# Kernel tuning notes

Hardware: AMD Instinct MI355X
Metric: run time of the kernel (lower is better)

## Reference

```python
import jax, jax.numpy as jnp
import numpy as np

S = 7                # feature map size
A = 12               # anchors per cell
N = S * S * A        # 588 total anchors
ANCHOR_SCALES = [0.3, 0.5, 0.7, 0.9]
ANCHOR_RATIOS = [0.7, 1.0, 1.3]
CONF_THR = 0.3
NMS_THR = 0.5
MAX_DET = 100
BN_EPS = 1e-5
DN = ('NCHW', 'OIHW', 'NCHW')


def _anchors():
    g = (jnp.arange(S, dtype=jnp.float32) + 0.5) / S
    cx, cy = jnp.meshgrid(g, g, indexing='ij')
    centers = jnp.stack([cx, cy], -1).reshape(-1, 2)                 # [49,2]
    sc = jnp.asarray(ANCHOR_SCALES, jnp.float32)[:, None]
    rt = jnp.sqrt(jnp.asarray(ANCHOR_RATIOS, jnp.float32))[None, :]
    ws = (sc * rt).reshape(-1)
    hs = (sc / rt).reshape(-1)
    deltas = jnp.stack([-ws, -hs, ws, hs], -1) * 0.5                 # [12,4]
    return (jnp.concatenate([centers, centers], -1)[:, None, :] + deltas[None]).reshape(-1, 4)


def _conv(x, w, b, pad):
    y = jax.lax.conv_general_dilated(x, w, (1, 1), [(pad, pad), (pad, pad)], dimension_numbers=DN)
    return y + b[None, :, None, None]


def _bn_relu(x, g, be, mu, var):
    inv = g * jax.lax.rsqrt(var + BN_EPS)
    return jax.nn.relu(x * inv[None, :, None, None] + (be - mu * inv)[None, :, None, None])


def _decode(box_pred, anchors):
    ac = (anchors[:, :2] + anchors[:, 2:]) * 0.5
    asz = anchors[:, 2:] - anchors[:, :2]
    pc = box_pred[..., :2] * asz + ac
    ps = jnp.exp(box_pred[..., 2:]) * asz
    return jnp.concatenate([pc - ps * 0.5, pc + ps * 0.5], -1)


def _iou(b):
    area = (b[:, 2] - b[:, 0]) * (b[:, 3] - b[:, 1])
    lt = jnp.maximum(b[:, None, :2], b[None, :, :2])
    rb = jnp.minimum(b[:, None, 2:], b[None, :, 2:])
    wh = jnp.clip(rb - lt, 0.0)
    inter = wh[..., 0] * wh[..., 1]
    return inter / (area[:, None] + area[None, :] - inter + 1e-9)


def _nms_single(boxes, scores):
    # greedy NMS, fixed-shape: sort by score, sequentially suppress, pad to MAX_DET
    order = jnp.argsort(-scores)
    bs = boxes[order]
    ss = scores[order]
    vs = ss > CONF_THR
    iou = _iou(bs)
    idx = jnp.arange(N)

    def body(suppr, i):
        keep = vs[i] & jnp.logical_not(suppr[i])
        suppr = suppr | (keep & (iou[i] > NMS_THR) & (idx > i))
        return suppr, keep

    _, keep = jax.lax.scan(body, jnp.zeros((N,), bool), idx)
    kept = jnp.where(keep, ss, -1.0)           # scores in (0,1), -1 is a safe sentinel
    top_s, top_i = jax.lax.top_k(kept, MAX_DET)
    valid = top_s > 0.0
    out_b = jnp.where(valid[:, None], bs[top_i], 0.0)
    out_s = jnp.where(valid, top_s, 0.0)
    return jnp.concatenate([out_b, out_s[:, None], valid.astype(jnp.float32)[:, None]], -1)


def _forward(features, w1, b1, g1, be1, mu1, var1, w2, b2, g2, be2, mu2, var2,
             w3, b3, g3, be3, mu3, var3, w4, b4, g4, be4, mu4, var4,
             w_cls, b_cls, w_box, b_box):
    x = _bn_relu(_conv(features, w1, b1, 0), g1, be1, mu1, var1)   # fpn 1x1
    x = _bn_relu(_conv(x, w2, b2, 1), g2, be2, mu2, var2)          # fpn 3x3
    x = _bn_relu(_conv(x, w3, b3, 1), g3, be3, mu3, var3)          # det_conv 1
    x = _bn_relu(_conv(x, w4, b4, 1), g4, be4, mu4, var4)          # det_conv 2
    B = features.shape[0]
    box = _conv(x, w_box, b_box, 1).transpose(0, 2, 3, 1).reshape(B, -1, 4)
    conf = jax.nn.sigmoid(_conv(x, w_cls, b_cls, 1)).transpose(0, 2, 3, 1).reshape(B, -1)
    boxes = _decode(box, _anchors())
    return jax.vmap(_nms_single)(boxes, conf)   # [B, MAX_DET, 6] = box(4)+score+valid


def setup_inputs() -> dict:
    key = jax.random.key(0)
    ks = iter(jax.random.split(key, 64))
    B = 256
    d = {'features': jax.random.normal(next(ks), (B, 512, S, S), jnp.float32)}
    for n, o, i, k in [('1', 256, 512, 1), ('2', 256, 256, 3), ('3', 256, 256, 3), ('4', 256, 256, 3)]:
        d['w' + n] = 0.01 * jax.random.normal(next(ks), (o, i, k, k), jnp.float32)
        d['b' + n] = jnp.zeros((o,), jnp.float32)
        d['g' + n] = 1.0 + 0.1 * jax.random.normal(next(ks), (o,), jnp.float32)
        d['be' + n] = 0.05 * jax.random.normal(next(ks), (o,), jnp.float32)
        d['mu' + n] = 0.1 * jax.random.normal(next(ks), (o,), jnp.float32)
        d['var' + n] = jax.random.uniform(next(ks), (o,), jnp.float32, 0.5, 1.5)
    d['w_cls'] = 0.01 * jax.random.normal(next(ks), (A, 256, 3, 3), jnp.float32)
    d['b_cls'] = jnp.zeros((A,), jnp.float32)
    d['w_box'] = 0.01 * jax.random.normal(next(ks), (4 * A, 256, 3, 3), jnp.float32)
    d['b_box'] = jnp.zeros((4 * A,), jnp.float32)
    return d


def reference(features, w1, b1, g1, be1, mu1, var1, w2, b2, g2, be2, mu2, var2,
              w3, b3, g3, be3, mu3, var3, w4, b4, g4, be4, mu4, var4,
              w_cls, b_cls, w_box, b_box):
    return _forward(features, w1, b1, g1, be1, mu1, var1, w2, b2, g2, be2, mu2, var2,
                    w3, b3, g3, be3, mu3, var3, w4, b4, g4, be4, mu4, var4,
                    w_cls, b_cls, w_box, b_box)
```

## Files before the change

kernel.cpp:

```cpp
#include <hip/hip_runtime.h>
#include <cmath>
#include <cstdint>

#define NPOS 49
#define NANCH 588

__global__ void transpose_all(
    const float* __restrict__ w1, const float* __restrict__ w2,
    const float* __restrict__ w3, const float* __restrict__ w4,
    const float* __restrict__ wb, const float* __restrict__ wc,
    float* __restrict__ w1t, float* __restrict__ w2t, float* __restrict__ w3t,
    float* __restrict__ w4t, float* __restrict__ wbt, float* __restrict__ wct) {
  int idx = blockIdx.x * blockDim.x + threadIdx.x;
  if (idx < 131072) {
    int o = idx / 512, c = idx % 512;
    w1t[((c >> 2) * 256 + o) * 4 + (c & 3)] = w1[idx];
    return;
  }
  idx -= 131072;
  if (idx < 589824) { int o = idx / 2304, ck = idx % 2304; w2t[ck * 256 + o] = w2[idx]; return; }
  idx -= 589824;
  if (idx < 589824) { int o = idx / 2304, ck = idx % 2304; w3t[ck * 256 + o] = w3[idx]; return; }
  idx -= 589824;
  if (idx < 589824) { int o = idx / 2304, ck = idx % 2304; w4t[ck * 256 + o] = w4[idx]; return; }
  idx -= 589824;
  if (idx < 110592) { int o = idx / 2304, ck = idx % 2304; wbt[ck * 48 + o] = wb[idx]; return; }
  idx -= 110592;
  if (idx < 27648)  { int o = idx / 2304, ck = idx % 2304; wct[ck * 12 + o] = wc[idx]; return; }
}

__global__ __launch_bounds__(512, 2) void conv1x1_bn(
    const float* __restrict__ wt_f, const float* __restrict__ in,
    const float* __restrict__ bias, const float* __restrict__ gg,
    const float* __restrict__ be, const float* __restrict__ mu,
    const float* __restrict__ var, float* __restrict__ out) {
  __shared__ float smem[256 * 52];
  const int blk = blockIdx.x, t = threadIdx.x;
  const int b = blk >> 1, oh = blk & 1;
  const int o = t & 127, cg = t >> 7;
  const int og = oh * 128 + o;
  const float* inb = in + (size_t)b * (512 * NPOS);
  const float4* wq = (const float4*)wt_f;
  float acc[NPOS];
#pragma unroll
  for (int p = 0; p < NPOS; ++p) acc[p] = 0.f;
  for (int h = 0; h < 2; ++h) {
    __syncthreads();
    const int q0 = h * 64 + cg * 16;
    float4 wcur = wq[q0 * 256 + og];
    for (int i = t; i < 256 * NPOS; i += 512) {
      int c = i / NPOS, p = i - c * NPOS;
      smem[c * 52 + p] = inb[(h * 256 + c) * NPOS + p];
    }
    __syncthreads();
    for (int q = q0; q < q0 + 16; ++q) {
      int nq = (q + 1 < q0 + 16) ? q + 1 : q;
      float4 wnxt = wq[nq * 256 + og];
      const int clbase = (q - h * 64) * 4;
#pragma unroll
      for (int j = 0; j < 4; ++j) {
        float wv = (j == 0) ? wcur.x : (j == 1) ? wcur.y : (j == 2) ? wcur.z : wcur.w;
        const float4* tr = (const float4*)(smem + (clbase + j) * 52);
#pragma unroll
        for (int jj = 0; jj < 12; ++jj) {
          float4 qv = tr[jj];
          acc[4 * jj + 0] = fmaf(wv, qv.x, acc[4 * jj + 0]);
          acc[4 * jj + 1] = fmaf(wv, qv.y, acc[4 * jj + 1]);
          acc[4 * jj + 2] = fmaf(wv, qv.z, acc[4 * jj + 2]);
          acc[4 * jj + 3] = fmaf(wv, qv.w, acc[4 * jj + 3]);
        }
        acc[48] = fmaf(wv, smem[(clbase + j) * 52 + 48], acc[48]);
      }
      wcur = wnxt;
    }
  }
  __syncthreads();
  float* P0 = smem;
  float* P1 = smem + 6272;
  if (cg == 1) { for (int p = 0; p < NPOS; ++p) P0[o * NPOS + p] = acc[p]; }
  if (cg == 3) { for (int p = 0; p < NPOS; ++p) P1[o * NPOS + p] = acc[p]; }
  __syncthreads();
  if (cg == 0) { for (int p = 0; p < NPOS; ++p) acc[p] += P0[o * NPOS + p]; }
  if (cg == 2) { for (int p = 0; p < NPOS; ++p) acc[p] += P1[o * NPOS + p]; }
  __syncthreads();
  if (cg == 2) { for (int p = 0; p < NPOS; ++p) P0[o * NPOS + p] = acc[p]; }
  __syncthreads();
  if (cg == 0) {
    float scale = gg[og] / sqrtf(var[og] + 1e-5f);
    float add = (bias[og] - mu[og]) * scale + be[og];
#pragma unroll
    for (int p = 0; p < NPOS; ++p) {
      float v = (acc[p] + P0[o * NPOS + p]) * scale + add;
      P1[o * NPOS + p] = v > 0.f ? v : 0.f;
    }
  }
  __syncthreads();
  float* outb = out + (size_t)b * (256 * NPOS) + oh * (128 * NPOS);
  for (int i = t; i < 128 * NPOS; i += 512) outb[i] = P1[i];
}

#define LOADROW(dst, base, rr)                                          \
  do {                                                                  \
    const float4* q4_ = (const float4*)((base) + (rr) * 12);            \
    float4 q0_ = q4_[0], q1_ = q4_[1], q2_ = q4_[2];                    \
    dst[0] = q0_.x; dst[1] = q0_.y; dst[2] = q0_.z; dst[3] = q0_.w;     \
    dst[4] = q1_.x; dst[5] = q1_.y; dst[6] = q1_.z; dst[7] = q1_.w;     \
    dst[8] = q2_.x;                                                     \
  } while (0)

__global__ __launch_bounds__(512, 2) void conv3x3_bn(
    const float* __restrict__ in, const float* __restrict__ wt,
    const float* __restrict__ bias, const float* __restrict__ gg,
    const float* __restrict__ be, const float* __restrict__ mu,
    const float* __restrict__ var, float* __restrict__ out) {
  __shared__ float smem[128 * 108];
  const int blk = blockIdx.x, t = threadIdx.x;
  const int b = blk >> 1, oh = blk & 1;
  const int o = t & 127, cg = t >> 7;
  const int og = oh * 128 + o;
  const float* inb = in + (size_t)b * (256 * NPOS);
  for (int i = t; i < 128 * 108; i += 512) smem[i] = 0.f;
  float acc[NPOS];
#pragma unroll
  for (int p = 0; p < NPOS; ++p) acc[p] = 0.f;
  for (int h = 0; h < 2; ++h) {
    __syncthreads();
    const int cb = h * 128 + cg * 32;
    float wc_[9];
#pragma unroll
    for (int k = 0; k < 9; ++k) wc_[k] = wt[(cb * 9 + k) * 256 + og];
    for (int i = t; i < 128 * NPOS; i += 512) {
      int c = i / NPOS, p = i - c * NPOS, y = p / 7, x = p - y * 7;
      smem[c * 108 + (y + 1) * 12 + (x + 1)] = inb[(h * 128 + c) * NPOS + p];
    }
    __syncthreads();
    for (int cl = 0; cl < 32; ++cl) {
      const int c = cb + cl;
      const int cn = (cl + 1 < 32) ? c + 1 : c;
      float wn_[9];
#pragma unroll
      for (int k = 0; k < 9; ++k) wn_[k] = wt[(cn * 9 + k) * 256 + og];
      const float* tb = smem + (cg * 32 + cl) * 108;
      float R[3][9];
      LOADROW(R[0], tb, 0);
      LOADROW(R[1], tb, 1);
#pragma unroll
      for (int y = 0; y < 7; ++y) {
        LOADROW(R[(y + 2) % 3], tb, y + 2);
        const float* r0 = R[y % 3];
        const float* r1 = R[(y + 1) % 3];
        const float* r2 = R[(y + 2) % 3];
#pragma unroll
        for (int x = 0; x < 7; ++x) {
          float s = acc[y * 7 + x];
          s = fmaf(wc_[0], r0[x], s);
          s = fmaf(wc_[1], r0[x + 1], s);
          s = fmaf(wc_[2], r0[x + 2], s);
          s = fmaf(wc_[3], r1[x], s);
          s = fmaf(wc_[4], r1[x + 1], s);
          s = fmaf(wc_[5], r1[x + 2], s);
          s = fmaf(wc_[6], r2[x], s);
          s = fmaf(wc_[7], r2[x + 1], s);
          s = fmaf(wc_[8], r2[x + 2], s);
          acc[y * 7 + x] = s;
        }
      }
#pragma unroll
      for (int k = 0; k < 9; ++k) wc_[k] = wn_[k];
    }
  }
  __syncthreads();
  float* P0 = smem;
  float* P1 = smem + 6272;
  if (cg == 1) { for (int p = 0; p < NPOS; ++p) P0[o * NPOS + p] = acc[p]; }
  if (cg == 3) { for (int p = 0; p < NPOS; ++p) P1[o * NPOS + p] = acc[p]; }
  __syncthreads();
  if (cg == 0) { for (int p = 0; p < NPOS; ++p) acc[p] += P0[o * NPOS + p]; }
  if (cg == 2) { for (int p = 0; p < NPOS; ++p) acc[p] += P1[o * NPOS + p]; }
  __syncthreads();
  if (cg == 2) { for (int p = 0; p < NPOS; ++p) P0[o * NPOS + p] = acc[p]; }
  __syncthreads();
  if (cg == 0) {
    float scale = gg[og] / sqrtf(var[og] + 1e-5f);
    float add = (bias[og] - mu[og]) * scale + be[og];
#pragma unroll
    for (int p = 0; p < NPOS; ++p) {
      float v = (acc[p] + P0[o * NPOS + p]) * scale + add;
      P1[o * NPOS + p] = v > 0.f ? v : 0.f;
    }
  }
  __syncthreads();
  float* outb = out + (size_t)b * (256 * NPOS) + oh * (128 * NPOS);
  for (int i = t; i < 128 * NPOS; i += 512) outb[i] = P1[i];
}

__global__ __launch_bounds__(512, 2) void heads_decode(
    const float* __restrict__ in, const float* __restrict__ wbt,
    const float* __restrict__ wct, const float* __restrict__ bb,
    const float* __restrict__ bc, float* __restrict__ BXg,
    float* __restrict__ SCg) {
  __shared__ float smem[256 * 108];
  const int b = blockIdx.x, t = threadIdx.x;
  for (int i = t; i < 256 * 108; i += 512) smem[i] = 0.f;
  __syncthreads();
  const float* inb = in + (size_t)b * (256 * NPOS);
  for (int i = t; i < 256 * NPOS; i += 512) {
    int c = i / NPOS, p = i - c * NPOS, y = p / 7, x = p - y * 7;
    smem[c * 108 + (y + 1) * 12 + (x + 1)] = inb[i];
  }
  __syncthreads();
  float acc[NPOS];
#pragma unroll
  for (int p = 0; p < NPOS; ++p) acc[p] = 0.f;
  int o = 0, cg = 0;
  if (t < 480) {
    o = t % 60; cg = t / 60;
    const float* wbase; int wstr;
    if (o < 48) { wbase = wbt + o; wstr = 48; }
    else        { wbase = wct + (o - 48); wstr = 12; }
    const int c0 = cg * 32;
    float wc_[9];
#pragma unroll
    for (int k = 0; k < 9; ++k) wc_[k] = wbase[(c0 * 9 + k) * wstr];
    for (int c = c0; c < c0 + 32; ++c) {
      int cn = (c + 1 < c0 + 32) ? c + 1 : c;
      float wn_[9];
#pragma unroll
      for (int k = 0; k < 9; ++k) wn_[k] = wbase[(cn * 9 + k) * wstr];
      const float* tb = smem + c * 108;
      float R[3][9];
      LOADROW(R[0], tb, 0);
      LOADROW(R[1], tb, 1);
#pragma unroll
      for (int y = 0; y < 7; ++y) {
        LOADROW(R[(y + 2) % 3], tb, y + 2);
        const float* r0 = R[y % 3];
        const float* r1 = R[(y + 1) % 3];
        const float* r2 = R[(y + 2) % 3];
#pragma unroll
        for (int x = 0; x < 7; ++x) {
          float s = acc[y * 7 + x];
          s = fmaf(wc_[0], r0[x], s);
          s = fmaf(wc_[1], r0[x + 1], s);
          s = fmaf(wc_[2], r0[x + 2], s);
          s = fmaf(wc_[3], r1[x], s);
          s = fmaf(wc_[4], r1[x + 1], s);
          s = fmaf(wc_[5], r1[x + 2], s);
          s = fmaf(wc_[6], r2[x], s);
          s = fmaf(wc_[7], r2[x + 1], s);
          s = fmaf(wc_[8], r2[x + 2], s);
          acc[y * 7 + x] = s;
        }
      }
#pragma unroll
      for (int k = 0; k < 9; ++k) wc_[k] = wn_[k];
    }
  }
  __syncthreads();
  float* part = smem;
  float* H = smem + 7 * 2940;
  if (t < 480 && cg > 0) {
#pragma unroll
    for (int p = 0; p < NPOS; ++p) part[(cg - 1) * 2940 + o * NPOS + p] = acc[p];
  }
  __syncthreads();
  if (t < 60) {
    float bsum = (o < 48) ? bb[o] : bc[o - 48];
#pragma unroll
    for (int p = 0; p < NPOS; ++p) {
      float v = acc[p] + bsum;
      for (int g = 0; g < 7; ++g) v += part[g * 2940 + o * NPOS + p];
      H[o * NPOS + p] = v;
    }
  }
  __syncthreads();
  const float scl[4] = {0.3f, 0.5f, 0.7f, 0.9f};
  const float rat[3] = {0.7f, 1.0f, 1.3f};
  for (int n = t; n < NANCH; n += 512) {
    int p = n / 12, a = n - p * 12;
    int ph = p / 7, pw = p - ph * 7;
    float cx = (ph + 0.5f) / 7.0f;
    float cy = (pw + 0.5f) / 7.0f;
    int s = a / 3, r = a - s * 3;
    float rt = sqrtf(rat[r]);
    float wsz = scl[s] * rt, hsz = scl[s] / rt;
    float x1 = cx + (-wsz) * 0.5f, y1 = cy + (-hsz) * 0.5f;
    float x2 = cx + wsz * 0.5f,    y2 = cy + hsz * 0.5f;
    float acx = (x1 + x2) * 0.5f,  acy = (y1 + y2) * 0.5f;
    float asx = x2 - x1,           asy = y2 - y1;
    float bp0 = H[(a * 4 + 0) * NPOS + p];
    float bp1 = H[(a * 4 + 1) * NPOS + p];
    float bp2 = H[(a * 4 + 2) * NPOS + p];
    float bp3 = H[(a * 4 + 3) * NPOS + p];
    float pcx = bp0 * asx + acx;
    float pcy = bp1 * asy + acy;
    float psx = expf(bp2) * asx;
    float psy = expf(bp3) * asy;
    float* bx = BXg + (size_t)b * (NANCH * 4) + n * 4;
    bx[0] = pcx - psx * 0.5f;
    bx[1] = pcy - psy * 0.5f;
    bx[2] = pcx + psx * 0.5f;
    bx[3] = pcy + psy * 0.5f;
    float lg = H[(48 + a) * NPOS + p];
    SCg[(size_t)b * NANCH + n] = 1.0f / (1.0f + expf(-lg));
  }
}

__device__ inline unsigned long long shfl64(unsigned long long v, int lane) {
  int lo = __shfl((int)(unsigned)(v & 0xffffffffULL), lane, 64);
  int hi = __shfl((int)(unsigned)(v >> 32), lane, 64);
  return ((unsigned long long)(unsigned)hi << 32) | (unsigned)lo;
}

__global__ __launch_bounds__(512, 4) void nms_kernel(
    const float* __restrict__ BXg, const float* __restrict__ SCg,
    float* __restrict__ out) {
  __shared__ float smem[16576];
  unsigned long long* KEY = (unsigned long long*)smem;
  float* SB  = smem + 1176;
  float* SSc = smem + 3528;
  float* AR  = smem + 4116;
  unsigned long long* ADJ = (unsigned long long*)(smem + 4704);
  int* KEEP = (int*)(smem + 16464);
  int* CNT  = (int*)(smem + 16564);
  const int b = blockIdx.x, t = threadIdx.x;
  const float* scb = SCg + (size_t)b * NANCH;
  const float4* bxb = (const float4*)(BXg + (size_t)b * (NANCH * 4));
  for (int i = t; i < NANCH; i += 512) {
    unsigned u = __float_as_uint(scb[i]);
    u = (u & 0x80000000u) ? ~u : (u | 0x80000000u);
    u = ~u;
    KEY[i] = ((unsigned long long)u << 32) | (unsigned)i;
  }
  __syncthreads();
  for (int i = t; i < NANCH; i += 512) {
    unsigned long long k = KEY[i];
    int rank = 0;
    for (int j = 0; j < NANCH; ++j) rank += (KEY[j] < k) ? 1 : 0;
    float4 bx = bxb[i];
    ((float4*)SB)[rank] = bx;
    SSc[rank] = scb[i];
    AR[rank] = (bx.z - bx.x) * (bx.w - bx.y);
  }
  __syncthreads();
  const float4* SB4 = (const float4*)SB;
  for (int task = t; task < NANCH * 10; task += 512) {
    int i = task % NANCH, w = task / NANCH;
    float4 a = SB4[i];
    float aar = AR[i];
    int jbase = w * 64;
    int jend = NANCH - jbase; if (jend > 64) jend = 64;
    unsigned long long bits = 0;
    for (int bi = 0; bi < jend; ++bi) {
      int j = jbase + bi;
      float4 bb = SB4[j];
      float ltx = fmaxf(a.x, bb.x), lty = fmaxf(a.y, bb.y);
      float rbx = fminf(a.z, bb.z), rby = fminf(a.w, bb.w);
      float wx = rbx - ltx; wx = wx > 0.f ? wx : 0.f;
      float wy = rby - lty; wy = wy > 0.f ? wy : 0.f;
      float inter = wx * wy;
      float iou = inter / (aar + AR[j] - inter + 1e-9f);
      if (iou > 0.5f) bits |= (1ULL << bi);
    }
    ADJ[i * 10 + w] = bits;
  }
  __syncthreads();
  if (t < 64) {
    unsigned long long valid = 0, supp = 0;
    if (t < 10) {
      int jbase = t * 64;
      int jend = NANCH - jbase; if (jend > 64) jend = 64;
      for (int k = 0; k < jend; ++k)
        valid |= (unsigned long long)(SSc[jbase + k] > 0.3f ? 1 : 0) << k;
    }
    int cnt = 0;
    for (int w = 0; w < 10 && cnt < 100; ++w) {
      unsigned long long cur = shfl64(valid, w) & ~shfl64(supp, w);
      while (cur && cnt < 100) {
        int bpos = (int)__builtin_ctzll(cur);
        int i = w * 64 + bpos;
        if (t == 0) KEEP[cnt] = i;
        cnt++;
        unsigned long long a = (t < 10) ? ADJ[i * 10 + t] : 0ULL;
        if (t < w) a = 0ULL;
        else if (t == w) a &= ~((2ULL << bpos) - 1ULL);
        supp |= a;
        unsigned long long aw = shfl64(a, w);
        cur &= ~aw;
        cur &= ~(1ULL << bpos);
      }
    }
    if (t == 0) *CNT = cnt;
  }
  __syncthreads();
  int cnt = *CNT;
  if (t < 100) {
    float4 bx = make_float4(0.f, 0.f, 0.f, 0.f);
    float s = 0.f, vld = 0.f;
    if (t < cnt) {
      int i = KEEP[t];
      bx = SB4[i];
      s = SSc[i];
      vld = 1.f;
    }
    float* ob = out + (size_t)b * 600 + t * 6;
    ob[0] = bx.x; ob[1] = bx.y; ob[2] = bx.z; ob[3] = bx.w;
    ob[4] = s;    ob[5] = vld;
  }
}

extern "C" void kernel_launch(void* const* d_in, const int* in_sizes, int n_in,
                              void* d_out, int out_size, void* d_ws, size_t ws_size,
                              hipStream_t stream) {
  const float* feat = (const float*)d_in[0];
  const float* w1  = (const float*)d_in[1];
  const float* b1  = (const float*)d_in[2];
  const float* g1  = (const float*)d_in[3];
  const float* be1 = (const float*)d_in[4];
  const float* mu1 = (const float*)d_in[5];
  const float* v1  = (const float*)d_in[6];
  const float* w2  = (const float*)d_in[7];
  const float* b2  = (const float*)d_in[8];
  const float* g2  = (const float*)d_in[9];
  const float* be2 = (const float*)d_in[10];
  const float* mu2 = (const float*)d_in[11];
  const float* v2  = (const float*)d_in[12];
  const float* w3  = (const float*)d_in[13];
  const float* b3  = (const float*)d_in[14];
  const float* g3  = (const float*)d_in[15];
  const float* be3 = (const float*)d_in[16];
  const float* mu3 = (const float*)d_in[17];
  const float* v3  = (const float*)d_in[18];
  const float* w4  = (const float*)d_in[19];
  const float* b4  = (const float*)d_in[20];
  const float* g4  = (const float*)d_in[21];
  const float* be4 = (const float*)d_in[22];
  const float* mu4 = (const float*)d_in[23];
  const float* v4  = (const float*)d_in[24];
  const float* wcls = (const float*)d_in[25];
  const float* bcls = (const float*)d_in[26];
  const float* wbox = (const float*)d_in[27];
  const float* bbox = (const float*)d_in[28];

  const int B = in_sizes[0] / (512 * NPOS);
  float* ws  = (float*)d_ws;
  size_t xsz = (size_t)B * 256 * NPOS;
  float* xa  = ws;
  float* xb  = xa + xsz;
  float* w1t = xb + xsz;
  float* w2t = w1t + 131072;
  float* w3t = w2t + 589824;
  float* w4t = w3t + 589824;
  float* wbt = w4t + 589824;
  float* wct = wbt + 110592;
  float* BXg = wct + 27648;
  float* SCg = BXg + (size_t)B * (NANCH * 4);

  transpose_all<<<(2038784 + 255) / 256, 256, 0, stream>>>(
      w1, w2, w3, w4, wbox, wcls, w1t, w2t, w3t, w4t, wbt, wct);
  conv1x1_bn<<<2 * B, 512, 0, stream>>>(w1t, feat, b1, g1, be1, mu1, v1, xa);
  conv3x3_bn<<<2 * B, 512, 0, stream>>>(xa, w2t, b2, g2, be2, mu2, v2, xb);
  conv3x3_bn<<<2 * B, 512, 0, stream>>>(xb, w3t, b3, g3, be3, mu3, v3, xa);
  conv3x3_bn<<<2 * B, 512, 0, stream>>>(xa, w4t, b4, g4, be4, mu4, v4, xb);
  heads_decode<<<B, 512, 0, stream>>>(xb, wbt, wct, bbox, bcls, BXg, SCg);
  nms_kernel<<<B, 512, 0, stream>>>(BXg, SCg, (float*)d_out);
}
```

Baseline: 958.5 us.

## Compute all 256 output channels per block with two accumulators per thread

Each conv block now handles one whole image (all 256 output channels) instead of half, so every thread keeps two 49-element accumulator sets and reuses each shared-memory input read for two output channels. Each image's input is staged into LDS once rather than once per half-block, and the 3x3 weights are relaid out into 12-float padded rows so they load as float4. In exchange the grid is halved, register use roughly doubles (launch bounds drop to 1 block per CU), and LDS per block doubles, which lowers occupancy and parallelism at small batch sizes.

```diff
diff --git a/kernel.cpp b/kernel.cpp
--- a/kernel.cpp
+++ b/kernel.cpp
@@ -18,85 +18,118 @@
     return;
   }
   idx -= 131072;
-  if (idx < 589824) { int o = idx / 2304, ck = idx % 2304; w2t[ck * 256 + o] = w2[idx]; return; }
+  if (idx < 589824) {
+    int o = idx / 2304, ck = idx % 2304, c = ck / 9, k = ck - c * 9;
+    w2t[(c * 256 + o) * 12 + k] = w2[idx]; return;
+  }
   idx -= 589824;
-  if (idx < 589824) { int o = idx / 2304, ck = idx % 2304; w3t[ck * 256 + o] = w3[idx]; return; }
+  if (idx < 589824) {
+    int o = idx / 2304, ck = idx % 2304, c = ck / 9, k = ck - c * 9;
+    w3t[(c * 256 + o) * 12 + k] = w3[idx]; return;
+  }
   idx -= 589824;
-  if (idx < 589824) { int o = idx / 2304, ck = idx % 2304; w4t[ck * 256 + o] = w4[idx]; return; }
+  if (idx < 589824) {
+    int o = idx / 2304, ck = idx % 2304, c = ck / 9, k = ck - c * 9;
+    w4t[(c * 256 + o) * 12 + k] = w4[idx]; return;
+  }
   idx -= 589824;
   if (idx < 110592) { int o = idx / 2304, ck = idx % 2304; wbt[ck * 48 + o] = wb[idx]; return; }
   idx -= 110592;
   if (idx < 27648)  { int o = idx / 2304, ck = idx % 2304; wct[ck * 12 + o] = wc[idx]; return; }
 }
 
-__global__ __launch_bounds__(512, 2) void conv1x1_bn(
-    const float* __restrict__ wt_f, const float* __restrict__ in,
+__global__ __launch_bounds__(512, 1) void conv1x1_bn(
+    const float* __restrict__ in, const float* __restrict__ wt_f,
     const float* __restrict__ bias, const float* __restrict__ gg,
     const float* __restrict__ be, const float* __restrict__ mu,
     const float* __restrict__ var, float* __restrict__ out) {
-  __shared__ float smem[256 * 52];
-  const int blk = blockIdx.x, t = threadIdx.x;
-  const int b = blk >> 1, oh = blk & 1;
-  const int o = t & 127, cg = t >> 7;
-  const int og = oh * 128 + o;
+  __shared__ float smem[512 * 52];
+  const int b = blockIdx.x, t = threadIdx.x;
+  const int slot = t & 127, cg = t >> 7;
+  const int o0 = slot, o1 = slot + 128;
   const float* inb = in + (size_t)b * (512 * NPOS);
   const float4* wq = (const float4*)wt_f;
-  float acc[NPOS];
-#pragma unroll
-  for (int p = 0; p < NPOS; ++p) acc[p] = 0.f;
-  for (int h = 0; h < 2; ++h) {
-    __syncthreads();
-    const int q0 = h * 64 + cg * 16;
-    float4 wcur = wq[q0 * 256 + og];
-    for (int i = t; i < 256 * NPOS; i += 512) {
-      int c = i / NPOS, p = i - c * NPOS;
-      smem[c * 52 + p] = inb[(h * 256 + c) * NPOS + p];
-    }
-    __syncthreads();
-    for (int q = q0; q < q0 + 16; ++q) {
-      int nq = (q + 1 < q0 + 16) ? q + 1 : q;
-      float4 wnxt = wq[nq * 256 + og];
-      const int clbase = (q - h * 64) * 4;
-#pragma unroll
-      for (int j = 0; j < 4; ++j) {
-        float wv = (j == 0) ? wcur.x : (j == 1) ? wcur.y : (j == 2) ? wcur.z : wcur.w;
-        const float4* tr = (const float4*)(smem + (clbase + j) * 52);
-#pragma unroll
-        for (int jj = 0; jj < 12; ++jj) {
-          float4 qv = tr[jj];
-          acc[4 * jj + 0] = fmaf(wv, qv.x, acc[4 * jj + 0]);
-          acc[4 * jj + 1] = fmaf(wv, qv.y, acc[4 * jj + 1]);
-          acc[4 * jj + 2] = fmaf(wv, qv.z, acc[4 * jj + 2]);
-          acc[4 * jj + 3] = fmaf(wv, qv.w, acc[4 * jj + 3]);
-        }
-        acc[48] = fmaf(wv, smem[(clbase + j) * 52 + 48], acc[48]);
+  const int q0 = cg * 32;
+  float4 wca = wq[q0 * 256 + o0];
+  float4 wcb = wq[q0 * 256 + o1];
+  for (int i = t; i < 512 * NPOS; i += 512) {
+    int c = i / NPOS, p = i - c * NPOS;
+    smem[c * 52 + p] = inb[i];
+  }
+  float acc0[NPOS], acc1[NPOS];
+#pragma unroll
+  for (int p = 0; p < NPOS; ++p) { acc0[p] = 0.f; acc1[p] = 0.f; }
+  __syncthreads();
+  for (int q = q0; q < q0 + 32; ++q) {
+    int nq = (q + 1 < q0 + 32) ? q + 1 : q;
+    float4 wna = wq[nq * 256 + o0];
+    float4 wnb = wq[nq * 256 + o1];
+#pragma unroll
+    for (int j = 0; j < 4; ++j) {
+      float wa = (j == 0) ? wca.x : (j == 1) ? wca.y : (j == 2) ? wca.z : wca.w;
+      float wb2 = (j == 0) ? wcb.x : (j == 1) ? wcb.y : (j == 2) ? wcb.z : wcb.w;
+      const float* row = smem + (q * 4 + j) * 52;
+      const float4* tr = (const float4*)row;
+#pragma unroll
+      for (int jj = 0; jj < 12; ++jj) {
+        float4 qv = tr[jj];
+        acc0[4 * jj + 0] = fmaf(wa, qv.x, acc0[4 * jj + 0]);
+        acc0[4 * jj + 1] = fmaf(wa, qv.y, acc0[4 * jj + 1]);
+        acc0[4 * jj + 2] = fmaf(wa, qv.z, acc0[4 * jj + 2]);
+        acc0[4 * jj + 3] = fmaf(wa, qv.w, acc0[4 * jj + 3]);
+        acc1[4 * jj + 0] = fmaf(wb2, qv.x, acc1[4 * jj + 0]);
+        acc1[4 * jj + 1] = fmaf(wb2, qv.y, acc1[4 * jj + 1]);
+        acc1[4 * jj + 2] = fmaf(wb2, qv.z, acc1[4 * jj + 2]);
+        acc1[4 * jj + 3] = fmaf(wb2, qv.w, acc1[4 * jj + 3]);
       }
-      wcur = wnxt;
-    }
+      float s48 = row[48];
+      acc0[48] = fmaf(wa, s48, acc0[48]);
+      acc1[48] = fmaf(wb2, s48, acc1[48]);
+    }
+    wca = wna; wcb = wnb;
   }
   __syncthreads();
   float* P0 = smem;
-  float* P1 = smem + 6272;
-  if (cg == 1) { for (int p = 0; p < NPOS; ++p) P0[o * NPOS + p] = acc[p]; }
-  if (cg == 3) { for (int p = 0; p < NPOS; ++p) P1[o * NPOS + p] = acc[p]; }
-  __syncthreads();
-  if (cg == 0) { for (int p = 0; p < NPOS; ++p) acc[p] += P0[o * NPOS + p]; }
-  if (cg == 2) { for (int p = 0; p < NPOS; ++p) acc[p] += P1[o * NPOS + p]; }
-  __syncthreads();
-  if (cg == 2) { for (int p = 0; p < NPOS; ++p) P0[o * NPOS + p] = acc[p]; }
+  float* P1 = smem + 12544;
+  if (cg == 1) {
+#pragma unroll
+    for (int p = 0; p < NPOS; ++p) { P0[(slot * 2 + 0) * NPOS + p] = acc0[p]; P0[(slot * 2 + 1) * NPOS + p] = acc1[p]; }
+  }
+  if (cg == 3) {
+#pragma unroll
+    for (int p = 0; p < NPOS; ++p) { P1[(slot * 2 + 0) * NPOS + p] = acc0[p]; P1[(slot * 2 + 1) * NPOS + p] = acc1[p]; }
+  }
   __syncthreads();
   if (cg == 0) {
-    float scale = gg[og] / sqrtf(var[og] + 1e-5f);
-    float add = (bias[og] - mu[og]) * scale + be[og];
+#pragma unroll
+    for (int p = 0; p < NPOS; ++p) { acc0[p] += P0[(slot * 2 + 0) * NPOS + p]; acc1[p] += P0[(slot * 2 + 1) * NPOS + p]; }
+  }
+  if (cg == 2) {
+#pragma unroll
+    for (int p = 0; p < NPOS; ++p) { acc0[p] += P1[(slot * 2 + 0) * NPOS + p]; acc1[p] += P1[(slot * 2 + 1) * NPOS + p]; }
+  }
+  __syncthreads();
+  if (cg == 2) {
+#pragma unroll
+    for (int p = 0; p < NPOS; ++p) { P0[(slot * 2 + 0) * NPOS + p] = acc0[p]; P0[(slot * 2 + 1) * NPOS + p] = acc1[p]; }
+  }
+  __syncthreads();
+  if (cg == 0) {
+    float sc0 = gg[o0] / sqrtf(var[o0] + 1e-5f);
+    float ad0 = (bias[o0] - mu[o0]) * sc0 + be[o0];
+    float sc1 = gg[o1] / sqrtf(var[o1] + 1e-5f);
+    float ad1 = (bias[o1] - mu[o1]) * sc1 + be[o1];
 #pragma unroll
     for (int p = 0; p < NPOS; ++p) {
-      float v = (acc[p] + P0[o * NPOS + p]) * scale + add;
-      P1[o * NPOS + p] = v > 0.f ? v : 0.f;
-    }
-  }
-  __syncthreads();
-  float* outb = out + (size_t)b * (256 * NPOS) + oh * (128 * NPOS);
-  for (int i = t; i < 128 * NPOS; i += 512) outb[i] = P1[i];
+      float v0 = (acc0[p] + P0[(slot * 2 + 0) * NPOS + p]) * sc0 + ad0;
+      float v1 = (acc1[p] + P0[(slot * 2 + 1) * NPOS + p]) * sc1 + ad1;
+      P1[o0 * NPOS + p] = v0 > 0.f ? v0 : 0.f;
+      P1[o1 * NPOS + p] = v1 > 0.f ? v1 : 0.f;
+    }
+  }
+  __syncthreads();
+  float* outb = out + (size_t)b * (256 * NPOS);
+  for (int i = t; i < 256 * NPOS; i += 512) outb[i] = P1[i];
 }
 
 #define LOADROW(dst, base, rr)                                          \
@@ -108,90 +141,125 @@
     dst[8] = q2_.x;                                                     \
   } while (0)
 
-__global__ __launch_bounds__(512, 2) void conv3x3_bn(
+__global__ __launch_bounds__(512, 1) void conv3x3_bn(
     const float* __restrict__ in, const float* __restrict__ wt,
     const float* __restrict__ bias, const float* __restrict__ gg,
     const float* __restrict__ be, const float* __restrict__ mu,
     const float* __restrict__ var, float* __restrict__ out) {
-  __shared__ float smem[128 * 108];
-  const int blk = blockIdx.x, t = threadIdx.x;
-  const int b = blk >> 1, oh = blk & 1;
-  const int o = t & 127, cg = t >> 7;
-  const int og = oh * 128 + o;
+  __shared__ float smem[256 * 108];
+  const int b = blockIdx.x, t = threadIdx.x;
+  const int slot = t & 127, cg = t >> 7;
+  const int o0 = slot, o1 = slot + 128;
   const float* inb = in + (size_t)b * (256 * NPOS);
-  for (int i = t; i < 128 * 108; i += 512) smem[i] = 0.f;
-  float acc[NPOS];
-#pragma unroll
-  for (int p = 0; p < NPOS; ++p) acc[p] = 0.f;
-  for (int h = 0; h < 2; ++h) {
-    __syncthreads();
-    const int cb = h * 128 + cg * 32;
-    float wc_[9];
-#pragma unroll
-    for (int k = 0; k < 9; ++k) wc_[k] = wt[(cb * 9 + k) * 256 + og];
-    for (int i = t; i < 128 * NPOS; i += 512) {
-      int c = i / NPOS, p = i - c * NPOS, y = p / 7, x = p - y * 7;
-      smem[c * 108 + (y + 1) * 12 + (x + 1)] = inb[(h * 128 + c) * NPOS + p];
-    }
-    __syncthreads();
-    for (int cl = 0; cl < 32; ++cl) {
-      const int c = cb + cl;
-      const int cn = (cl + 1 < 32) ? c + 1 : c;
-      float wn_[9];
-#pragma unroll
-      for (int k = 0; k < 9; ++k) wn_[k] = wt[(cn * 9 + k) * 256 + og];
-      const float* tb = smem + (cg * 32 + cl) * 108;
-      float R[3][9];
-      LOADROW(R[0], tb, 0);
-      LOADROW(R[1], tb, 1);
-#pragma unroll
-      for (int y = 0; y < 7; ++y) {
-        LOADROW(R[(y + 2) % 3], tb, y + 2);
-        const float* r0 = R[y % 3];
-        const float* r1 = R[(y + 1) % 3];
-        const float* r2 = R[(y + 2) % 3];
-#pragma unroll
-        for (int x = 0; x < 7; ++x) {
-          float s = acc[y * 7 + x];
-          s = fmaf(wc_[0], r0[x], s);
-          s = fmaf(wc_[1], r0[x + 1], s);
-          s = fmaf(wc_[2], r0[x + 2], s);
-          s = fmaf(wc_[3], r1[x], s);
-          s = fmaf(wc_[4], r1[x + 1], s);
-          s = fmaf(wc_[5], r1[x + 2], s);
-          s = fmaf(wc_[6], r2[x], s);
-          s = fmaf(wc_[7], r2[x + 1], s);
-          s = fmaf(wc_[8], r2[x + 2], s);
-          acc[y * 7 + x] = s;
-        }
+  float4* z4 = (float4*)smem;
+  for (int i = t; i < 6912; i += 512) z4[i] = make_float4(0.f, 0.f, 0.f, 0.f);
+  const int c0 = cg * 64;
+  const float4* wv4 = (const float4*)wt;
+  float4 wa0 = wv4[(c0 * 256 + o0) * 3 + 0];
+  float4 wa1 = wv4[(c0 * 256 + o0) * 3 + 1];
+  float4 wa2 = wv4[(c0 * 256 + o0) * 3 + 2];
+  float4 wb0 = wv4[(c0 * 256 + o1) * 3 + 0];
+  float4 wb1 = wv4[(c0 * 256 + o1) * 3 + 1];
+  float4 wb2 = wv4[(c0 * 256 + o1) * 3 + 2];
+  __syncthreads();
+  for (int i = t; i < 256 * NPOS; i += 512) {
+    int c = i / NPOS, p = i - c * NPOS, y = p / 7, x = p - y * 7;
+    smem[c * 108 + (y + 1) * 12 + (x + 1)] = inb[i];
+  }
+  float acc0[NPOS], acc1[NPOS];
+#pragma unroll
+  for (int p = 0; p < NPOS; ++p) { acc0[p] = 0.f; acc1[p] = 0.f; }
+  __syncthreads();
+  for (int cl = 0; cl < 64; ++cl) {
+    const int c = c0 + cl;
+    const int cn = (cl + 1 < 64) ? c + 1 : c;
+    float4 na0 = wv4[(cn * 256 + o0) * 3 + 0];
+    float4 na1 = wv4[(cn * 256 + o0) * 3 + 1];
+    float4 na2 = wv4[(cn * 256 + o0) * 3 + 2];
+    float4 nb0 = wv4[(cn * 256 + o1) * 3 + 0];
+    float4 nb1 = wv4[(cn * 256 + o1) * 3 + 1];
+    float4 nb2 = wv4[(cn * 256 + o1) * 3 + 2];
+    const float* tb = smem + c * 108;
+    float R[3][9];
+    LOADROW(R[0], tb, 0);
+    LOADROW(R[1], tb, 1);
+#pragma unroll
+    for (int y = 0; y < 7; ++y) {
+      LOADROW(R[(y + 2) % 3], tb, y + 2);
+      const float* r0 = R[y % 3];
+      const float* r1 = R[(y + 1) % 3];
+      const float* r2 = R[(y + 2) % 3];
+#pragma unroll
+      for (int x = 0; x < 7; ++x) {
+        float s0 = acc0[y * 7 + x];
+        s0 = fmaf(wa0.x, r0[x],     s0);
+        s0 = fmaf(wa0.y, r0[x + 1], s0);
+        s0 = fmaf(wa0.z, r0[x + 2], s0);
+        s0 = fmaf(wa0.w, r1[x],     s0);
+        s0 = fmaf(wa1.x, r1[x + 1], s0);
+        s0 = fmaf(wa1.y, r1[x + 2], s0);
+        s0 = fmaf(wa1.z, r2[x],     s0);
+        s0 = fmaf(wa1.w, r2[x + 1], s0);
+        s0 = fmaf(wa2.x, r2[x + 2], s0);
+        acc0[y * 7 + x] = s0;
+        float s1 = acc1[y * 7 + x];
+        s1 = fmaf(wb0.x, r0[x],     s1);
+        s1 = fmaf(wb0.y, r0[x + 1], s1);
+        s1 = fmaf(wb0.z, r0[x + 2], s1);
+        s1 = fmaf(wb0.w, r1[x],     s1);
+        s1 = fmaf(wb1.x, r1[x + 1], s1);
+        s1 = fmaf(wb1.y, r1[x + 2], s1);
+        s1 = fmaf(wb1.z, r2[x],     s1);
+        s1 = fmaf(wb1.w, r2[x + 1], s1);
+        s1 = fmaf(wb2.x, r2[x + 2], s1);
+        acc1[y * 7 + x] = s1;
       }
-#pragma unroll
-      for (int k = 0; k < 9; ++k) wc_[k] = wn_[k];
-    }
+    }
+    wa0 = na0; wa1 = na1; wa2 = na2;
+    wb0 = nb0; wb1 = nb1; wb2 = nb2;
   }
   __syncthreads();
   float* P0 = smem;
-  float* P1 = smem + 6272;
-  if (cg == 1) { for (int p = 0; p < NPOS; ++p) P0[o * NPOS + p] = acc[p]; }
-  if (cg == 3) { for (int p = 0; p < NPOS; ++p) P1[o * NPOS + p] = acc[p]; }
-  __syncthreads();
-  if (cg == 0) { for (int p = 0; p < NPOS; ++p) acc[p] += P0[o * NPOS + p]; }
-  if (cg == 2) { for (int p = 0; p < NPOS; ++p) acc[p] += P1[o * NPOS + p]; }
-  __syncthreads();
-  if (cg == 2) { for (int p = 0; p < NPOS; ++p) P0[o * NPOS + p] = acc[p]; }
+  float* P1 = smem + 12544;
+  if (cg == 1) {
+#pragma unroll
+    for (int p = 0; p < NPOS; ++p) { P0[(slot * 2 + 0) * NPOS + p] = acc0[p]; P0[(slot * 2 + 1) * NPOS + p] = acc1[p]; }
+  }
+  if (cg == 3) {
+#pragma unroll
+    for (int p = 0; p < NPOS; ++p) { P1[(slot * 2 + 0) * NPOS + p] = acc0[p]; P1[(slot * 2 + 1) * NPOS + p] = acc1[p]; }
+  }
   __syncthreads();
   if (cg == 0) {
-    float scale = gg[og] / sqrtf(var[og] + 1e-5f);
-    float add = (bias[og] - mu[og]) * scale + be[og];
+#pragma unroll
+    for (int p = 0; p < NPOS; ++p) { acc0[p] += P0[(slot * 2 + 0) * NPOS + p]; acc1[p] += P0[(slot * 2 + 1) * NPOS + p]; }
+  }
+  if (cg == 2) {
+#pragma unroll
+    for (int p = 0; p < NPOS; ++p) { acc0[p] += P1[(slot * 2 + 0) * NPOS + p]; acc1[p] += P1[(slot * 2 + 1) * NPOS + p]; }
+  }
+  __syncthreads();
+  if (cg == 2) {
+#pragma unroll
+    for (int p = 0; p < NPOS; ++p) { P0[(slot * 2 + 0) * NPOS + p] = acc0[p]; P0[(slot * 2 + 1) * NPOS + p] = acc1[p]; }
+  }
+  __syncthreads();
+  if (cg == 0) {
+    float sc0 = gg[o0] / sqrtf(var[o0] + 1e-5f);
+    float ad0 = (bias[o0] - mu[o0]) * sc0 + be[o0];
+    float sc1 = gg[o1] / sqrtf(var[o1] + 1e-5f);
+    float ad1 = (bias[o1] - mu[o1]) * sc1 + be[o1];
 #pragma unroll
     for (int p = 0; p < NPOS; ++p) {
-      float v = (acc[p] + P0[o * NPOS + p]) * scale + add;
-      P1[o * NPOS + p] = v > 0.f ? v : 0.f;
-    }
-  }
-  __syncthreads();
-  float* outb = out + (size_t)b * (256 * NPOS) + oh * (128 * NPOS);
-  for (int i = t; i < 128 * NPOS; i += 512) outb[i] = P1[i];
+      float v0 = (acc0[p] + P0[(slot * 2 + 0) * NPOS + p]) * sc0 + ad0;
+      float v1 = (acc1[p] + P0[(slot * 2 + 1) * NPOS + p]) * sc1 + ad1;
+      P1[o0 * NPOS + p] = v0 > 0.f ? v0 : 0.f;
+      P1[o1 * NPOS + p] = v1 > 0.f ? v1 : 0.f;
+    }
+  }
+  __syncthreads();
+  float* outb = out + (size_t)b * (256 * NPOS);
+  for (int i = t; i < 256 * NPOS; i += 512) outb[i] = P1[i];
 }
 
 __global__ __launch_bounds__(512, 2) void heads_decode(
@@ -449,19 +517,19 @@
   float* xb  = xa + xsz;
   float* w1t = xb + xsz;
   float* w2t = w1t + 131072;
-  float* w3t = w2t + 589824;
-  float* w4t = w3t + 589824;
-  float* wbt = w4t + 589824;
+  float* w3t = w2t + 786432;
+  float* w4t = w3t + 786432;
+  float* wbt = w4t + 786432;
   float* wct = wbt + 110592;
   float* BXg = wct + 27648;
   float* SCg = BXg + (size_t)B * (NANCH * 4);
 
   transpose_all<<<(2038784 + 255) / 256, 256, 0, stream>>>(
       w1, w2, w3, w4, wbox, wcls, w1t, w2t, w3t, w4t, wbt, wct);
-  conv1x1_bn<<<2 * B, 512, 0, stream>>>(w1t, feat, b1, g1, be1, mu1, v1, xa);
-  conv3x3_bn<<<2 * B, 512, 0, stream>>>(xa, w2t, b2, g2, be2, mu2, v2, xb);
-  conv3x3_bn<<<2 * B, 512, 0, stream>>>(xb, w3t, b3, g3, be3, mu3, v3, xa);
-  conv3x3_bn<<<2 * B, 512, 0, stream>>>(xa, w4t, b4, g4, be4, mu4, v4, xb);
+  conv1x1_bn<<<B, 512, 0, stream>>>(feat, w1t, b1, g1, be1, mu1, v1, xa);
+  conv3x3_bn<<<B, 512, 0, stream>>>(xa, w2t, b2, g2, be2, mu2, v2, xb);
+  conv3x3_bn<<<B, 512, 0, stream>>>(xb, w3t, b3, g3, be3, mu3, v3, xa);
+  conv3x3_bn<<<B, 512, 0, stream>>>(xa, w4t, b4, g4, be4, mu4, v4, xb);
   heads_decode<<<B, 512, 0, stream>>>(xb, wbt, wct, bbox, bcls, BXg, SCg);
   nms_kernel<<<B, 512, 0, stream>>>(BXg, SCg, (float*)d_out);
 }
```

After: 895.9 us. -6.5%, faster.
